# Kernel tuning notes

Measured on AMD Instinct MI355X. Metric: run time of the kernel, lower is better.

Reference implementation:

```python
import jax, jax.numpy as jnp
import numpy as np

B, L, D, H = 32, 1024, 1024, 1024

def setup_inputs() -> dict:
    key = jax.random.key(0)
    k1, k2, k3 = jax.random.split(key, 3)
    query = jax.random.normal(k1, (B, L, D), dtype=jnp.float32)
    keys = jax.random.normal(k2, (B, L, D), dtype=jnp.float32)
    # xavier_normal for Linear(D, H): std = sqrt(2/(D+H))
    W = jax.random.normal(k3, (H, D), dtype=jnp.float32) * np.sqrt(2.0 / (D + H)).astype(np.float32)
    b = jnp.zeros((H,), dtype=jnp.float32)
    return {"query": query, "keys": keys, "W": W, "b": b}

def reference(query, keys, W, b):
    # L2-normalize along feature dim (matches torch .norm(dim=-1, keepdim=True))
    qn = query / jnp.linalg.norm(query, axis=-1, keepdims=True)
    kn = keys / jnp.linalg.norm(keys, axis=-1, keepdims=True)
    # scores[b,i,j] = <kn[b,i], qn[b,j]>  ->  [B, Lk, Lq]
    scores = jnp.einsum('bid,bjd->bij', kn, qn)
    attn = jax.nn.softmax(scores, axis=-1)
    # bmm(attn, keys) then sum over batch -> [L, D]
    out = jnp.einsum('bij,bjd->id', attn, keys)
    x = jax.nn.relu(out @ W.T + b)
    return (x, attn)
```

## Files before the change

kernel.cpp:

```cpp
#include <hip/hip_runtime.h>
#include <hip/hip_bf16.h>

#define NBATCH 32
#define Ls 1024
#define Ds 1024
#define Hs 1024

typedef float f32x4 __attribute__((ext_vector_type(4)));
typedef __bf16 v8bf __attribute__((ext_vector_type(8)));
typedef unsigned short u16x8 __attribute__((ext_vector_type(8)));
typedef unsigned short u16x4 __attribute__((ext_vector_type(4)));
typedef __hip_bfloat16 bf16;

__device__ __forceinline__ float bfbits2f(unsigned short h) {
  unsigned u = ((unsigned)h) << 16;
  return __builtin_bit_cast(float, u);
}
__device__ __forceinline__ unsigned short f2b(float x) {
  return __builtin_bit_cast(unsigned short, __float2bfloat16(x));
}
__device__ __forceinline__ u16x8 pack8(const float4& a, const float4& b, float s) {
  u16x8 r;
  r[0] = f2b(a.x * s); r[1] = f2b(a.y * s); r[2] = f2b(a.z * s); r[3] = f2b(a.w * s);
  r[4] = f2b(b.x * s); r[5] = f2b(b.y * s); r[6] = f2b(b.z * s); r[7] = f2b(b.w * s);
  return r;
}

__global__ __launch_bounds__(256) void k_convert(const float* __restrict__ q,
                                                 const float* __restrict__ k,
                                                 bf16* __restrict__ qn,
                                                 bf16* __restrict__ kb,
                                                 float* __restrict__ invk) {
  const int w0 = ((int)blockIdx.x * 256 + (int)threadIdx.x) >> 6;
  const int lane = threadIdx.x & 63;
  #pragma unroll
  for (int it = 0; it < 2; ++it) {
    const size_t r0 = ((size_t)(it * 8192 + w0)) * 2;
    const float4* q0 = reinterpret_cast<const float4*>(q + r0 * Ds);
    const float4* k0 = reinterpret_cast<const float4*>(k + r0 * Ds);
    float4 qv[2][4], kv[2][4];
    #pragma unroll
    for (int rr = 0; rr < 2; ++rr)
      #pragma unroll
      for (int h = 0; h < 2; ++h) {
        qv[rr][h * 2 + 0] = q0[rr * 256 + h * 128 + lane * 2 + 0];
        qv[rr][h * 2 + 1] = q0[rr * 256 + h * 128 + lane * 2 + 1];
        kv[rr][h * 2 + 0] = k0[rr * 256 + h * 128 + lane * 2 + 0];
        kv[rr][h * 2 + 1] = k0[rr * 256 + h * 128 + lane * 2 + 1];
      }
    float sq0 = 0.f, sq1 = 0.f, sk0 = 0.f, sk1 = 0.f;
    #pragma unroll
    for (int p = 0; p < 4; ++p) {
      sq0 += qv[0][p].x*qv[0][p].x + qv[0][p].y*qv[0][p].y + qv[0][p].z*qv[0][p].z + qv[0][p].w*qv[0][p].w;
      sq1 += qv[1][p].x*qv[1][p].x + qv[1][p].y*qv[1][p].y + qv[1][p].z*qv[1][p].z + qv[1][p].w*qv[1][p].w;
      sk0 += kv[0][p].x*kv[0][p].x + kv[0][p].y*kv[0][p].y + kv[0][p].z*kv[0][p].z + kv[0][p].w*kv[0][p].w;
      sk1 += kv[1][p].x*kv[1][p].x + kv[1][p].y*kv[1][p].y + kv[1][p].z*kv[1][p].z + kv[1][p].w*kv[1][p].w;
    }
    #pragma unroll
    for (int o = 1; o < 64; o <<= 1) {
      sq0 += __shfl_xor(sq0, o); sq1 += __shfl_xor(sq1, o);
      sk0 += __shfl_xor(sk0, o); sk1 += __shfl_xor(sk1, o);
    }
    const float iq0 = 1.0f / sqrtf(sq0), iq1 = 1.0f / sqrtf(sq1);
    if (lane == 0) {
      invk[r0]     = 1.0f / sqrtf(sk0);
      invk[r0 + 1] = 1.0f / sqrtf(sk1);
    }
    u16x8* qo = reinterpret_cast<u16x8*>(qn + r0 * Ds);
    u16x8* ko = reinterpret_cast<u16x8*>(kb + r0 * Ds);
    qo[lane]        = pack8(qv[0][0], qv[0][1], iq0);
    qo[64 + lane]   = pack8(qv[0][2], qv[0][3], iq0);
    qo[128 + lane]  = pack8(qv[1][0], qv[1][1], iq1);
    qo[192 + lane]  = pack8(qv[1][2], qv[1][3], iq1);
    ko[lane]        = pack8(kv[0][0], kv[0][1], 1.0f);
    ko[64 + lane]   = pack8(kv[0][2], kv[0][3], 1.0f);
    ko[128 + lane]  = pack8(kv[1][0], kv[1][1], 1.0f);
    ko[192 + lane]  = pack8(kv[1][2], kv[1][3], 1.0f);
  }
}

__global__ __launch_bounds__(256) void k_transpose(const bf16* __restrict__ kb,
                                                   bf16* __restrict__ kT) {
  __shared__ float tile[64][65];
  const int b = blockIdx.z;
  const int d0 = blockIdx.x * 64, j0 = blockIdx.y * 64;
  const int t = threadIdx.x;
  const int jr = t >> 4;
  const int c4 = (t & 15) * 4;
  const bf16* src = kb + (size_t)b * Ls * Ds;
  #pragma unroll
  for (int rr = 0; rr < 4; ++rr) {
    const int j = jr + rr * 16;
    const u16x4 v = *reinterpret_cast<const u16x4*>(&src[(size_t)(j0 + j) * Ds + d0 + c4]);
    tile[j][c4 + 0] = bfbits2f(v[0]);
    tile[j][c4 + 1] = bfbits2f(v[1]);
    tile[j][c4 + 2] = bfbits2f(v[2]);
    tile[j][c4 + 3] = bfbits2f(v[3]);
  }
  __syncthreads();
  bf16* dst = kT + (size_t)b * Ds * Ls;
  #pragma unroll
  for (int rr = 0; rr < 4; ++rr) {
    const int d = jr + rr * 16;
    u16x4 o = { f2b(tile[c4 + 0][d]), f2b(tile[c4 + 1][d]),
                f2b(tile[c4 + 2][d]), f2b(tile[c4 + 3][d]) };
    *reinterpret_cast<u16x4*>(&dst[(size_t)(d0 + d) * Ls + j0 + c4]) = o;
  }
}

__global__ __launch_bounds__(256) void k_w2(const float* __restrict__ W,
                                            bf16* __restrict__ W2) {
  const size_t idx = (size_t)blockIdx.x * 256 + threadIdx.x;
  const size_t e0 = idx * 4;
  const size_t h = e0 >> 10, d = e0 & 1023;
  const float4 w = reinterpret_cast<const float4*>(W)[idx];
  u16x4 wh = { f2b(w.x), f2b(w.y), f2b(w.z), f2b(w.w) };
  u16x4 wl = { f2b(w.x - bfbits2f(wh[0])), f2b(w.y - bfbits2f(wh[1])),
               f2b(w.z - bfbits2f(wh[2])), f2b(w.w - bfbits2f(wh[3])) };
  bf16* row = W2 + h * 3072;
  *reinterpret_cast<u16x4*>(row + d) = wh;
  *reinterpret_cast<u16x4*>(row + 1024 + d) = wh;
  *reinterpret_cast<u16x4*>(row + 2048 + d) = wl;
}

template<int KT, int MODE>
__global__ __launch_bounds__(512) void k_gemm256(
    const bf16* __restrict__ A, const bf16* __restrict__ B,
    void* __restrict__ Cv, const float* __restrict__ scale,
    int lda, int ldb, int ldc, int nb,
    size_t sA, size_t sB, size_t zA, size_t zB, size_t zC, size_t zS)
{
  __shared__ bf16 lds[2][2][256 * 64];
  const int tid = threadIdx.x;
  const int lane = tid & 63;
  const int wid = tid >> 6;
  const int wr = wid >> 2;
  const int wc = wid & 3;
  const size_t m0 = (size_t)blockIdx.y * 256;
  const size_t n0 = (size_t)blockIdx.x * 256;
  const bf16* Az = A + (size_t)blockIdx.z * zA;
  const bf16* Bz = B + (size_t)blockIdx.z * zB;

  const int srow = tid >> 3;
  const int sslot = tid & 7;
  f32x4 acc[8][4] = {};

  auto stage = [&](int tt, int buf) {
    const int b = tt / KT;
    const int k0 = (tt - b * KT) * 64;
    const bf16* Abp = Az + (size_t)b * sA;
    const bf16* Bbp = Bz + (size_t)b * sB;
    #pragma unroll
    for (int c = 0; c < 4; ++c) {
      const int row = c * 64 + srow;
      const int ksl = (sslot ^ (row & 7)) * 8;
      __builtin_amdgcn_global_load_lds(
          (const __attribute__((address_space(1))) void*)(Abp + (m0 + row) * lda + k0 + ksl),
          (__attribute__((address_space(3))) void*)(&lds[buf][0][c * 4096 + tid * 8]), 16, 0, 0);
    }
    #pragma unroll
    for (int c = 0; c < 4; ++c) {
      const int row = c * 64 + srow;
      const int ksl = (sslot ^ (row & 7)) * 8;
      __builtin_amdgcn_global_load_lds(
          (const __attribute__((address_space(1))) void*)(Bbp + (n0 + row) * ldb + k0 + ksl),
          (__attribute__((address_space(3))) void*)(&lds[buf][1][c * 4096 + tid * 8]), 16, 0, 0);
    }
  };

  const int rsel = lane & 15, qd = lane >> 4;
  auto compute = [&](int buf) {
    const bf16* As = lds[buf][0];
    const bf16* Bs = lds[buf][1];
    v8bf bfrag[2][4];
    #pragma unroll
    for (int h = 0; h < 2; ++h)
      #pragma unroll
      for (int n = 0; n < 4; ++n) {
        const int r = wc * 64 + n * 16 + rsel;
        const int s = (h * 4 + qd) ^ (r & 7);
        bfrag[h][n] = *reinterpret_cast<const v8bf*>(
            reinterpret_cast<const char*>(Bs) + r * 128 + s * 16);
      }
    #pragma unroll
    for (int m = 0; m < 8; ++m) {
      const int r = wr * 128 + m * 16 + rsel;
      const int s0 = qd ^ (r & 7);
      const int s1 = (4 + qd) ^ (r & 7);
      const v8bf a0 = *reinterpret_cast<const v8bf*>(
          reinterpret_cast<const char*>(As) + r * 128 + s0 * 16);
      const v8bf a1 = *reinterpret_cast<const v8bf*>(
          reinterpret_cast<const char*>(As) + r * 128 + s1 * 16);
      #pragma unroll
      for (int n = 0; n < 4; ++n)
        acc[m][n] = __builtin_amdgcn_mfma_f32_16x16x32_bf16(a0, bfrag[0][n], acc[m][n], 0, 0, 0);
      #pragma unroll
      for (int n = 0; n < 4; ++n)
        acc[m][n] = __builtin_amdgcn_mfma_f32_16x16x32_bf16(a1, bfrag[1][n], acc[m][n], 0, 0, 0);
    }
  };

  const int T = KT * nb;
  stage(0, 0);
  for (int t = 0; t < T - 1; ++t) {
    __builtin_amdgcn_s_barrier();
    stage(t + 1, (t + 1) & 1);
    asm volatile("s_waitcnt vmcnt(8)" ::: "memory");
    __builtin_amdgcn_s_barrier();
    compute(t & 1);
  }
  asm volatile("s_waitcnt vmcnt(0)" ::: "memory");
  __builtin_amdgcn_s_barrier();
  compute((T - 1) & 1);

  if (MODE == 0) {
    float* Cz = (float*)Cv + (size_t)blockIdx.z * zC;
    #pragma unroll
    for (int m = 0; m < 8; ++m) {
      const size_t ri = m0 + wr * 128 + m * 16 + (size_t)((lane >> 4) * 4);
      #pragma unroll
      for (int n = 0; n < 4; ++n) {
        const size_t cj = n0 + wc * 64 + n * 16 + (lane & 15);
        #pragma unroll
        for (int r = 0; r < 4; ++r)
          Cz[(ri + r) * ldc + cj] = acc[m][n][r];
      }
    }
  } else {
    bf16* Cz = (bf16*)Cv + (size_t)blockIdx.z * zC;
    const float* Sz = scale + (size_t)blockIdx.z * zS;
    #pragma unroll
    for (int m = 0; m < 8; ++m) {
      const size_t ri = m0 + wr * 128 + m * 16 + (size_t)((lane >> 4) * 4);
      const float4 ik = *reinterpret_cast<const float4*>(Sz + ri);
      #pragma unroll
      for (int n = 0; n < 4; ++n) {
        const size_t cj = n0 + wc * 64 + n * 16 + (lane & 15);
        Cz[(ri + 0) * ldc + cj] = __float2bfloat16(acc[m][n][0] * ik.x);
        Cz[(ri + 1) * ldc + cj] = __float2bfloat16(acc[m][n][1] * ik.y);
        Cz[(ri + 2) * ldc + cj] = __float2bfloat16(acc[m][n][2] * ik.z);
        Cz[(ri + 3) * ldc + cj] = __float2bfloat16(acc[m][n][3] * ik.w);
      }
    }
  }
}

__global__ __launch_bounds__(256) void k_gemm_nt(
    const bf16* __restrict__ A, const bf16* __restrict__ B,
    float* __restrict__ C,
    int lda, int ldb, int ldc, int K,
    size_t zA, size_t zB, size_t zC)
{
  __shared__ bf16 As[128 * 32];
  __shared__ bf16 Bs[128 * 32];
  const int tid = threadIdx.x;
  const int lane = tid & 63;
  const int wc = (tid >> 6) & 1;
  const int wr = (tid >> 7) & 1;
  const size_t m0 = (size_t)blockIdx.y * 128;
  const size_t n0 = (size_t)blockIdx.x * 128;
  const bf16* Az = A + (size_t)blockIdx.z * zA;
  const bf16* Bz = B + (size_t)blockIdx.z * zB;
  float* Cz = C + (size_t)blockIdx.z * zC;
  f32x4 acc[4][4] = {};

  const int beta0 = tid * 16;
  const int row0 = tid >> 2;
  const int kk0 = ((tid & 3) ^ ((row0 >> 1) & 3)) * 8;
  const int sw = (((lane >> 4) ^ ((lane >> 1) & 3)) << 4);
  const int rsel = lane & 15;

  for (int k0 = 0; k0 < K; k0 += 32) {
    __syncthreads();
    __builtin_amdgcn_global_load_lds(
        (const __attribute__((address_space(1))) void*)(Az + (m0 + row0) * lda + (k0 + kk0)),
        (__attribute__((address_space(3))) void*)(&As[beta0 / 2]), 16, 0, 0);
    __builtin_amdgcn_global_load_lds(
        (const __attribute__((address_space(1))) void*)(Az + (m0 + row0 + 64) * lda + (k0 + kk0)),
        (__attribute__((address_space(3))) void*)(&As[beta0 / 2 + 2048]), 16, 0, 0);
    __builtin_amdgcn_global_load_lds(
        (const __attribute__((address_space(1))) void*)(Bz + (n0 + row0) * ldb + (k0 + kk0)),
        (__attribute__((address_space(3))) void*)(&Bs[beta0 / 2]), 16, 0, 0);
    __builtin_amdgcn_global_load_lds(
        (const __attribute__((address_space(1))) void*)(Bz + (n0 + row0 + 64) * ldb + (k0 + kk0)),
        (__attribute__((address_space(3))) void*)(&Bs[beta0 / 2 + 2048]), 16, 0, 0);
    __syncthreads();

    v8bf af[4], bg[4];
    #pragma unroll
    for (int m = 0; m < 4; ++m) {
      const int rA = wr * 64 + m * 16 + rsel;
      af[m] = *reinterpret_cast<const v8bf*>(reinterpret_cast<const char*>(As) + rA * 64 + sw);
      const int rB = wc * 64 + m * 16 + rsel;
      bg[m] = *reinterpret_cast<const v8bf*>(reinterpret_cast<const char*>(Bs) + rB * 64 + sw);
    }
    #pragma unroll
    for (int m = 0; m < 4; ++m)
      #pragma unroll
      for (int n = 0; n < 4; ++n)
        acc[m][n] = __builtin_amdgcn_mfma_f32_16x16x32_bf16(af[m], bg[n], acc[m][n], 0, 0, 0);
  }

  #pragma unroll
  for (int m = 0; m < 4; ++m) {
    const size_t ri = m0 + wr * 64 + m * 16 + ((lane >> 4) * 4);
    #pragma unroll
    for (int n = 0; n < 4; ++n) {
      const size_t cj = n0 + wc * 64 + n * 16 + (lane & 15);
      #pragma unroll
      for (int r = 0; r < 4; ++r)
        Cz[(ri + r) * ldc + cj] = acc[m][n][r];
    }
  }
}

__global__ __launch_bounds__(256) void k_softmax(const bf16* __restrict__ sc,
                                                 float* __restrict__ attn,
                                                 bf16* __restrict__ abf) {
  const int wave = ((int)blockIdx.x * 256 + (int)threadIdx.x) >> 6;
  const int lane = threadIdx.x & 63;
  for (int i = 0; i < 4; ++i) {
    const size_t row = (size_t)wave * 4 + i;
    const u16x8* sr = reinterpret_cast<const u16x8*>(sc + row * Ls);
    const u16x8 s0 = sr[lane], s1 = sr[lane + 64];
    float e[16];
    float ss = 0.f;
    #pragma unroll
    for (int j = 0; j < 8; ++j) { e[j] = __expf(bfbits2f(s0[j])); ss += e[j]; }
    #pragma unroll
    for (int j = 0; j < 8; ++j) { e[8 + j] = __expf(bfbits2f(s1[j])); ss += e[8 + j]; }
    #pragma unroll
    for (int o = 1; o < 64; o <<= 1) ss += __shfl_xor(ss, o);
    const float inv = 1.0f / ss;
    #pragma unroll
    for (int j = 0; j < 16; ++j) e[j] *= inv;
    float4* ar = reinterpret_cast<float4*>(attn + row * Ls);
    float4 a0 = {e[0], e[1], e[2], e[3]},   a1 = {e[4], e[5], e[6], e[7]};
    float4 a2 = {e[8], e[9], e[10], e[11]}, a3 = {e[12], e[13], e[14], e[15]};
    ar[lane * 2 + 0] = a0;  ar[lane * 2 + 1] = a1;
    ar[128 + lane * 2 + 0] = a2;  ar[128 + lane * 2 + 1] = a3;
    u16x8* ab8 = reinterpret_cast<u16x8*>(abf + row * Ls);
    u16x8 b0, b1;
    #pragma unroll
    for (int j = 0; j < 8; ++j) { b0[j] = f2b(e[j]); b1[j] = f2b(e[8 + j]); }
    ab8[lane] = b0;
    ab8[64 + lane] = b1;
  }
}

__global__ __launch_bounds__(256) void k_reduce(const float* __restrict__ part,
                                                bf16* __restrict__ A2) {
  const size_t idx = (size_t)blockIdx.x * 256 + threadIdx.x;
  float4 s = {0.f, 0.f, 0.f, 0.f};
  #pragma unroll
  for (int g = 0; g < 16; ++g) {
    const float4 p = reinterpret_cast<const float4*>(part + (size_t)g * (Ls * Ds))[idx];
    s.x += p.x; s.y += p.y; s.z += p.z; s.w += p.w;
  }
  const size_t e0 = idx * 4;
  const size_t i = e0 >> 10, d = e0 & 1023;
  u16x4 h = { f2b(s.x), f2b(s.y), f2b(s.z), f2b(s.w) };
  u16x4 l = { f2b(s.x - bfbits2f(h[0])), f2b(s.y - bfbits2f(h[1])),
              f2b(s.z - bfbits2f(h[2])), f2b(s.w - bfbits2f(h[3])) };
  bf16* row = A2 + i * 3072;
  *reinterpret_cast<u16x4*>(row + d) = h;
  *reinterpret_cast<u16x4*>(row + 1024 + d) = l;
  *reinterpret_cast<u16x4*>(row + 2048 + d) = h;
}

__global__ __launch_bounds__(256) void k_reduce2(const float* __restrict__ part2,
                                                 const float* __restrict__ bias,
                                                 float* __restrict__ xout) {
  const size_t idx = (size_t)blockIdx.x * 256 + threadIdx.x;
  float4 s = {0.f, 0.f, 0.f, 0.f};
  #pragma unroll
  for (int g = 0; g < 4; ++g) {
    const float4 p = reinterpret_cast<const float4*>(part2 + (size_t)g * (Ls * Hs))[idx];
    s.x += p.x; s.y += p.y; s.z += p.z; s.w += p.w;
  }
  const size_t h0 = (idx * 4) & 1023;
  const float4 bv = *reinterpret_cast<const float4*>(bias + h0);
  s.x = fmaxf(s.x + bv.x, 0.f); s.y = fmaxf(s.y + bv.y, 0.f);
  s.z = fmaxf(s.z + bv.z, 0.f); s.w = fmaxf(s.w + bv.w, 0.f);
  reinterpret_cast<float4*>(xout)[idx] = s;
}

extern "C" void kernel_launch(void* const* d_in, const int* in_sizes, int n_in,
                              void* d_out, int out_size, void* d_ws, size_t ws_size,
                              hipStream_t stream) {
  const float* q = (const float*)d_in[0];
  const float* k = (const float*)d_in[1];
  const float* W = (const float*)d_in[2];
  const float* bias = (const float*)d_in[3];
  float* xout = (float*)d_out;
  float* attn = (float*)d_out + (size_t)Ls * Hs;

  char* w = (char*)d_ws;
  bf16* qn    = (bf16*)w;
  bf16* kb    = (bf16*)(w + ((size_t)64 << 20));
  bf16* kT    = (bf16*)(w + ((size_t)128 << 20));
  bf16* sc_bf = (bf16*)(w + ((size_t)192 << 20));
  bf16* W2    = (bf16*)(w + ((size_t)256 << 20));
  bf16* A2    = (bf16*)(w + ((size_t)263 << 20));
  float* invk = (float*)(w + ((size_t)270 << 20));
  float* part  = (float*)kb;
  float* part2 = (float*)kT;
  bf16* abf = qn;

  k_convert<<<2048, 256, 0, stream>>>(q, k, qn, kb, invk);
  k_transpose<<<dim3(16, 16, NBATCH), 256, 0, stream>>>(kb, kT);
  k_w2<<<(Hs * Ds / 4) / 256, 256, 0, stream>>>(W, W2);

  k_gemm256<16, 1><<<dim3(4, 4, NBATCH), 512, 0, stream>>>(kb, qn, sc_bf, invk,
      Ds, Ds, Ls, 1,
      (size_t)Ls * Ds, (size_t)Ls * Ds,
      (size_t)Ls * Ds, (size_t)Ls * Ds, (size_t)Ls * Ls, (size_t)Ls);

  k_softmax<<<2048, 256, 0, stream>>>(sc_bf, attn, abf);

  k_gemm256<16, 0><<<dim3(4, 4, 16), 512, 0, stream>>>(abf, kT, part, nullptr,
      Ls, Ls, Ds, 2,
      (size_t)Ls * Ls, (size_t)Ls * Ds,
      (size_t)2 * Ls * Ls, (size_t)2 * Ls * Ds, (size_t)Ls * Ds, 0);

  k_reduce<<<(Ls * Ds / 4) / 256, 256, 0, stream>>>(part, A2);

  k_gemm_nt<<<dim3(8, 8, 4), 256, 0, stream>>>(A2, W2, part2,
      3072, 3072, Hs, 768, 768, 768, (size_t)Ls * Hs);

  k_reduce2<<<(Ls * Hs / 4) / 256, 256, 0, stream>>>(part2, bias, xout);
}
```

Before: 359.9 us.

## Fuse key conversion, norm, and transpose into one kernel reading fp32 keys

```diff
diff --git a/kernel.cpp b/kernel.cpp
--- a/kernel.cpp
+++ b/kernel.cpp
@@ -26,85 +26,93 @@
   return r;
 }
 
-__global__ __launch_bounds__(256) void k_convert(const float* __restrict__ q,
-                                                 const float* __restrict__ k,
-                                                 bf16* __restrict__ qn,
-                                                 bf16* __restrict__ kb,
-                                                 float* __restrict__ invk) {
+__global__ __launch_bounds__(256) void k_convq(const float* __restrict__ q,
+                                               bf16* __restrict__ qn) {
   const int w0 = ((int)blockIdx.x * 256 + (int)threadIdx.x) >> 6;
   const int lane = threadIdx.x & 63;
   #pragma unroll
   for (int it = 0; it < 2; ++it) {
     const size_t r0 = ((size_t)(it * 8192 + w0)) * 2;
     const float4* q0 = reinterpret_cast<const float4*>(q + r0 * Ds);
-    const float4* k0 = reinterpret_cast<const float4*>(k + r0 * Ds);
-    float4 qv[2][4], kv[2][4];
+    float4 qv[2][4];
     #pragma unroll
     for (int rr = 0; rr < 2; ++rr)
       #pragma unroll
       for (int h = 0; h < 2; ++h) {
         qv[rr][h * 2 + 0] = q0[rr * 256 + h * 128 + lane * 2 + 0];
         qv[rr][h * 2 + 1] = q0[rr * 256 + h * 128 + lane * 2 + 1];
-        kv[rr][h * 2 + 0] = k0[rr * 256 + h * 128 + lane * 2 + 0];
-        kv[rr][h * 2 + 1] = k0[rr * 256 + h * 128 + lane * 2 + 1];
       }
-    float sq0 = 0.f, sq1 = 0.f, sk0 = 0.f, sk1 = 0.f;
+    float sq0 = 0.f, sq1 = 0.f;
     #pragma unroll
     for (int p = 0; p < 4; ++p) {
       sq0 += qv[0][p].x*qv[0][p].x + qv[0][p].y*qv[0][p].y + qv[0][p].z*qv[0][p].z + qv[0][p].w*qv[0][p].w;
       sq1 += qv[1][p].x*qv[1][p].x + qv[1][p].y*qv[1][p].y + qv[1][p].z*qv[1][p].z + qv[1][p].w*qv[1][p].w;
-      sk0 += kv[0][p].x*kv[0][p].x + kv[0][p].y*kv[0][p].y + kv[0][p].z*kv[0][p].z + kv[0][p].w*kv[0][p].w;
-      sk1 += kv[1][p].x*kv[1][p].x + kv[1][p].y*kv[1][p].y + kv[1][p].z*kv[1][p].z + kv[1][p].w*kv[1][p].w;
-    }
-    #pragma unroll
-    for (int o = 1; o < 64; o <<= 1) {
-      sq0 += __shfl_xor(sq0, o); sq1 += __shfl_xor(sq1, o);
-      sk0 += __shfl_xor(sk0, o); sk1 += __shfl_xor(sk1, o);
-    }
+    }
+    #pragma unroll
+    for (int o = 1; o < 64; o <<= 1) { sq0 += __shfl_xor(sq0, o); sq1 += __shfl_xor(sq1, o); }
     const float iq0 = 1.0f / sqrtf(sq0), iq1 = 1.0f / sqrtf(sq1);
-    if (lane == 0) {
-      invk[r0]     = 1.0f / sqrtf(sk0);
-      invk[r0 + 1] = 1.0f / sqrtf(sk1);
-    }
     u16x8* qo = reinterpret_cast<u16x8*>(qn + r0 * Ds);
-    u16x8* ko = reinterpret_cast<u16x8*>(kb + r0 * Ds);
     qo[lane]        = pack8(qv[0][0], qv[0][1], iq0);
     qo[64 + lane]   = pack8(qv[0][2], qv[0][3], iq0);
     qo[128 + lane]  = pack8(qv[1][0], qv[1][1], iq1);
     qo[192 + lane]  = pack8(qv[1][2], qv[1][3], iq1);
-    ko[lane]        = pack8(kv[0][0], kv[0][1], 1.0f);
-    ko[64 + lane]   = pack8(kv[0][2], kv[0][3], 1.0f);
-    ko[128 + lane]  = pack8(kv[1][0], kv[1][1], 1.0f);
-    ko[192 + lane]  = pack8(kv[1][2], kv[1][3], 1.0f);
-  }
-}
-
-__global__ __launch_bounds__(256) void k_transpose(const bf16* __restrict__ kb,
-                                                   bf16* __restrict__ kT) {
+  }
+}
+
+__global__ __launch_bounds__(256) void k_convkT(const float* __restrict__ k,
+                                                bf16* __restrict__ kb,
+                                                bf16* __restrict__ kT,
+                                                float* __restrict__ invk) {
   __shared__ float tile[64][65];
-  const int b = blockIdx.z;
-  const int d0 = blockIdx.x * 64, j0 = blockIdx.y * 64;
+  __shared__ float red[4][16][16];
+  const int b = blockIdx.y;
+  const int j0 = blockIdx.x * 64;
   const int t = threadIdx.x;
   const int jr = t >> 4;
-  const int c4 = (t & 15) * 4;
-  const bf16* src = kb + (size_t)b * Ls * Ds;
+  const int cg = t & 15;
+  const int c4 = cg * 4;
+  const float* src = k + (size_t)b * Ls * Ds + (size_t)j0 * Ds;
+  bf16* kbd = kb + (size_t)b * Ls * Ds + (size_t)j0 * Ds;
+  bf16* kTd = kT + (size_t)b * Ds * Ls + j0;
+  float ssq[4] = {0.f, 0.f, 0.f, 0.f};
+
+  for (int dc = 0; dc < 16; ++dc) {
+    const int d0 = dc * 64;
+    float4 v[4];
+    #pragma unroll
+    for (int rr = 0; rr < 4; ++rr) {
+      const int j = jr + rr * 16;
+      v[rr] = *reinterpret_cast<const float4*>(&src[(size_t)j * Ds + d0 + c4]);
+      ssq[rr] += v[rr].x*v[rr].x + v[rr].y*v[rr].y + v[rr].z*v[rr].z + v[rr].w*v[rr].w;
+      u16x4 o = { f2b(v[rr].x), f2b(v[rr].y), f2b(v[rr].z), f2b(v[rr].w) };
+      *reinterpret_cast<u16x4*>(&kbd[(size_t)j * Ds + d0 + c4]) = o;
+    }
+    __syncthreads();
+    #pragma unroll
+    for (int rr = 0; rr < 4; ++rr) {
+      const int j = jr + rr * 16;
+      tile[j][c4 + 0] = v[rr].x; tile[j][c4 + 1] = v[rr].y;
+      tile[j][c4 + 2] = v[rr].z; tile[j][c4 + 3] = v[rr].w;
+    }
+    __syncthreads();
+    #pragma unroll
+    for (int rr = 0; rr < 4; ++rr) {
+      const int dd = jr + rr * 16;
+      u16x4 o = { f2b(tile[c4 + 0][dd]), f2b(tile[c4 + 1][dd]),
+                  f2b(tile[c4 + 2][dd]), f2b(tile[c4 + 3][dd]) };
+      *reinterpret_cast<u16x4*>(&kTd[(size_t)(d0 + dd) * Ls + c4]) = o;
+    }
+  }
+
   #pragma unroll
-  for (int rr = 0; rr < 4; ++rr) {
-    const int j = jr + rr * 16;
-    const u16x4 v = *reinterpret_cast<const u16x4*>(&src[(size_t)(j0 + j) * Ds + d0 + c4]);
-    tile[j][c4 + 0] = bfbits2f(v[0]);
-    tile[j][c4 + 1] = bfbits2f(v[1]);
-    tile[j][c4 + 2] = bfbits2f(v[2]);
-    tile[j][c4 + 3] = bfbits2f(v[3]);
-  }
+  for (int rr = 0; rr < 4; ++rr) red[rr][jr][cg] = ssq[rr];
   __syncthreads();
-  bf16* dst = kT + (size_t)b * Ds * Ls;
-  #pragma unroll
-  for (int rr = 0; rr < 4; ++rr) {
-    const int d = jr + rr * 16;
-    u16x4 o = { f2b(tile[c4 + 0][d]), f2b(tile[c4 + 1][d]),
-                f2b(tile[c4 + 2][d]), f2b(tile[c4 + 3][d]) };
-    *reinterpret_cast<u16x4*>(&dst[(size_t)(d0 + d) * Ls + j0 + c4]) = o;
+  if (t < 64) {
+    const int r = (t & 15) + (t >> 4) * 16;
+    float s = 0.f;
+    #pragma unroll
+    for (int c = 0; c < 16; ++c) s += red[t >> 4][t & 15][c];
+    invk[(size_t)b * Ls + j0 + r] = 1.0f / sqrtf(s);
   }
 }
 
@@ -407,8 +415,8 @@
   float* part2 = (float*)kT;
   bf16* abf = qn;
 
-  k_convert<<<2048, 256, 0, stream>>>(q, k, qn, kb, invk);
-  k_transpose<<<dim3(16, 16, NBATCH), 256, 0, stream>>>(kb, kT);
+  k_convq<<<2048, 256, 0, stream>>>(q, qn);
+  k_convkT<<<dim3(16, NBATCH), 256, 0, stream>>>(k, kb, kT, invk);
   k_w2<<<(Hs * Ds / 4) / 256, 256, 0, stream>>>(W, W2);
 
   k_gemm256<16, 1><<<dim3(4, 4, NBATCH), 512, 0, stream>>>(kb, qn, sc_bf, invk,
```

Result: no change. 357.5 us (-0.7%).
